# Kernel tuning notes

Hardware: AMD Instinct MI355X
Metric: run time of the kernel (lower is better)

## Reference

```python
import jax, jax.numpy as jnp
import numpy as np

SOFTCAP = 30.0

def setup_inputs() -> dict:
    key = jax.random.key(0)
    ks = jax.random.split(key, 5)
    T, D, F, E = 8192, 2048, 4096, 8
    s_in = 1.0 / np.sqrt(D)
    s_mid = 1.0 / np.sqrt(F)
    return {
        "hidden_states": jax.random.normal(ks[0], (T, D), jnp.float32),
        "gate_w": jax.random.normal(ks[1], (D, E), jnp.float32) * s_in,
        "w_gate": jax.random.normal(ks[2], (E, D, F), jnp.float32) * s_in,
        "w_up": jax.random.normal(ks[3], (E, D, F), jnp.float32) * s_in,
        "w_down": jax.random.normal(ks[4], (E, F, D), jnp.float32) * s_mid,
        "top_k": 2,
    }

def reference(hidden_states, gate_w, w_gate, w_up, w_down, top_k):
    x = hidden_states
    T = x.shape[0]
    # --- router: fp32 gate, tanh softcap, softmax ---
    logits = x.astype(jnp.float32) @ gate_w                      # [T, E]
    logits = jnp.tanh(logits / SOFTCAP) * SOFTCAP
    probs = jax.nn.softmax(logits, axis=-1)                      # [T, E]
    # --- top-k selection (weights are the softmax probs, no renorm) ---
    weights, idx = jax.lax.top_k(probs, top_k)                   # [T, k]
    combine = jnp.zeros_like(probs).at[jnp.arange(T)[:, None], idx].set(
        weights.astype(probs.dtype))                              # [T, E]
    combine = combine.astype(x.dtype)
    # --- expert MLPs: gelu(x@w_gate) * (x@w_up) @ w_down, scan over E ---
    def step(acc, ewts):
        wg, wu, wd, c = ewts                                     # [D,F],[D,F],[F,D],[T]
        h = jax.nn.gelu(x @ wg) * (x @ wu)                       # [T, F]
        return acc + c[:, None] * (h @ wd), None
    out, _ = jax.lax.scan(step, jnp.zeros_like(x),
                          (w_gate, w_up, w_down, combine.T))
    return out
```

## Files before the change

### kernel.cpp

```cpp
#include <hip/hip_runtime.h>
#include <hip/hip_bf16.h>
#include <cstdint>
#include <cstddef>

#define TNUM 8192
#define DDIM 2048
#define FDIM 4096
#define NEXP 8

typedef __attribute__((ext_vector_type(4))) float f32x4;
typedef __attribute__((ext_vector_type(4))) unsigned u32x4;
typedef __attribute__((ext_vector_type(8))) short s16x8;
typedef __attribute__((ext_vector_type(8))) __bf16 bf16x8v;

__device__ inline f32x4 mfma16(s16x8 a, s16x8 b, f32x4 c) {
  return __builtin_amdgcn_mfma_f32_16x16x32_bf16(
      __builtin_bit_cast(bf16x8v, a), __builtin_bit_cast(bf16x8v, b), c, 0, 0, 0);
}

__device__ inline unsigned short bf16r(float f) {
  union { float f; unsigned u; } x; x.f = f;
  unsigned r = x.u + 0x7fffu + ((x.u >> 16) & 1u);
  return (unsigned short)(r >> 16);
}

__device__ inline unsigned pk2(float a, float b) {
  __hip_bfloat162 h = __float22bfloat162_rn(make_float2(a, b));
  unsigned r;
  __builtin_memcpy(&r, &h, 4);
  return r;
}

__device__ inline int swz16(int row, int b) {
  return (row << 7) + (b ^ ((row & 7) << 4));
}

typedef const __attribute__((address_space(1))) void* gp_t;
typedef __attribute__((address_space(3))) void* lp_t;
__device__ inline void gl16(const void* g, void* l) {
  __builtin_amdgcn_global_load_lds((gp_t)g, (lp_t)l, 16, 0, 0);
}

#define FENCE asm volatile("" ::: "memory")

__global__ __launch_bounds__(256) void k_router(
    const float* __restrict__ x, const float* __restrict__ gw,
    int* __restrict__ top_idx, float* __restrict__ top_w, int* __restrict__ counts) {
  __shared__ float gwT[NEXP][DDIM];
  const int tid = threadIdx.x;
  for (int i = tid; i < NEXP * DDIM; i += 256) {
    int d = i >> 3, e = i & 7;
    gwT[e][d] = gw[i];
  }
  __syncthreads();
  const int lane = tid & 63;
  const int t = blockIdx.x * 4 + (tid >> 6);
  const float4* xr = (const float4*)(x + (size_t)t * DDIM);
  double acc[NEXP];
#pragma unroll
  for (int e = 0; e < NEXP; e++) acc[e] = 0.0;
  for (int d4 = lane; d4 < DDIM / 4; d4 += 64) {
    float4 xv = xr[d4];
#pragma unroll
    for (int e = 0; e < NEXP; e++) {
      float4 gv = *(const float4*)&gwT[e][d4 * 4];
      acc[e] += (double)xv.x * gv.x + (double)xv.y * gv.y +
                (double)xv.z * gv.z + (double)xv.w * gv.w;
    }
  }
#pragma unroll
  for (int e = 0; e < NEXP; e++) {
    double v = acc[e];
#pragma unroll
    for (int s = 32; s > 0; s >>= 1) v += __shfl_xor(v, s);
    acc[e] = v;
  }
  if (lane == 0) {
    int i0 = 0; double b0 = acc[0];
#pragma unroll
    for (int e = 1; e < NEXP; e++) if (acc[e] > b0) { b0 = acc[e]; i0 = e; }
    int i1 = (i0 == 0) ? 1 : 0; double b1 = acc[i1];
#pragma unroll
    for (int e = 0; e < NEXP; e++) {
      if (e == i0 || e == i1) continue;
      if (acc[e] > b1) { b1 = acc[e]; i1 = e; }
    }
    float lc[NEXP]; float mx = -1e30f;
#pragma unroll
    for (int e = 0; e < NEXP; e++) {
      lc[e] = tanhf((float)(acc[e] * (1.0 / 30.0))) * 30.0f;
      mx = lc[e] > mx ? lc[e] : mx;
    }
    float s = 0.0f;
#pragma unroll
    for (int e = 0; e < NEXP; e++) { lc[e] = expf(lc[e] - mx); s += lc[e]; }
    float inv = 1.0f / s;
    top_idx[t * 2] = i0; top_idx[t * 2 + 1] = i1;
    top_w[t * 2] = lc[i0] * inv; top_w[t * 2 + 1] = lc[i1] * inv;
    atomicAdd(&counts[i0], 1);
    atomicAdd(&counts[i1], 1);
  }
}

__global__ void k_scan(const int* __restrict__ counts, int* __restrict__ offs,
                       int* __restrict__ cursor) {
  if (threadIdx.x == 0) {
    int s = 0;
    for (int e = 0; e < NEXP; e++) { offs[e] = s; cursor[e] = s; s += counts[e]; }
    offs[NEXP] = s;
  }
}

__global__ void k_scatter(const int* __restrict__ top_idx, const float* __restrict__ top_w,
                          int* __restrict__ cursor, int* __restrict__ perm_tok,
                          float* __restrict__ perm_w) {
  int t = blockIdx.x * 256 + threadIdx.x;
#pragma unroll
  for (int k = 0; k < 2; k++) {
    int e = top_idx[t * 2 + k];
    int pos = atomicAdd(&cursor[e], 1);
    perm_tok[pos] = t;
    perm_w[pos] = top_w[t * 2 + k];
  }
}

__global__ void k_cast(const float* __restrict__ x, unsigned short* __restrict__ xb) {
  size_t i = ((size_t)blockIdx.x * 256 + threadIdx.x) * 8;
  f32x4 a = *(const f32x4*)(x + i);
  f32x4 b = *(const f32x4*)(x + i + 4);
  u32x4 v;
  v[0] = pk2(a[0], a[1]); v[1] = pk2(a[2], a[3]);
  v[2] = pk2(b[0], b[1]); v[3] = pk2(b[2], b[3]);
  *(u32x4*)(xb + i) = v;
}

__global__ __launch_bounds__(256) void k_convT(
    const float* __restrict__ src, unsigned short* __restrict__ dst,
    int K, int N, int cmap) {
  __shared__ char ct[8192];
  const int e = blockIdx.z;
  const float* src_e = src + (size_t)e * K * N;
  const int nout = cmap ? 2 * N : N;
  unsigned short* dst_e = dst + (size_t)e * nout * K;
  const int k0 = blockIdx.y * 64, n0 = blockIdx.x * 64;
  const int tid = threadIdx.x;
#pragma unroll
  for (int i = 0; i < 4; i++) {
    int idx = tid + i * 256;
    int kr = idx >> 4, f4 = idx & 15;
    f32x4 v = *(const f32x4*)(src_e + (size_t)(k0 + kr) * N + n0 + f4 * 4);
#pragma unroll
    for (int j = 0; j < 4; j++) {
      int n = f4 * 4 + j;
      *(unsigned short*)(ct + n * 128 + ((kr * 2) ^ ((n & 7) << 4))) = bf16r(v[j]);
    }
  }
  __syncthreads();
#pragma unroll
  for (int i = 0; i < 2; i++) {
    int s = tid + i * 256;
    int n = s >> 3, ks = s & 7;
    int gn = n0 + n;
    int cd = cmap ? (((gn >> 4) << 5) + (gn & 15) + (cmap == 2 ? 16 : 0)) : gn;
    s16x8 val = *(const s16x8*)(ct + n * 128 + ((ks * 16) ^ ((n & 7) << 4)));
    *(s16x8*)(dst_e + (size_t)cd * K + k0 + ks * 8) = val;
  }
}

#define PHASE(MIH, NIH, BUF)                                                   \
  {                                                                            \
    char* Ab_ = lds + (BUF) * 65536;                                           \
    char* Bb_ = Ab_ + 32768;                                                   \
    __builtin_amdgcn_s_setprio(1);                                             \
    _Pragma("unroll") for (int kk = 0; kk < 2; kk++) {                         \
      s16x8 b0_ = *(const s16x8*)(Bb_ +                                        \
          swz16(wc * 64 + (NIH) * 32 + l15, kk * 64 + lk * 16));               \
      s16x8 b1_ = *(const s16x8*)(Bb_ +                                        \
          swz16(wc * 64 + (NIH) * 32 + 16 + l15, kk * 64 + lk * 16));          \
      _Pragma("unroll") for (int mi = 0; mi < 4; mi++) {                       \
        s16x8 a_ = *(const s16x8*)(Ab_ +                                       \
            swz16(wr * 128 + (MIH) * 64 + mi * 16 + l15, kk * 64 + lk * 16));  \
        acc[(MIH) * 4 + mi][(NIH) * 2 + 0] =                                   \
            mfma16(a_, b0_, acc[(MIH) * 4 + mi][(NIH) * 2 + 0]);               \
        acc[(MIH) * 4 + mi][(NIH) * 2 + 1] =                                   \
            mfma16(a_, b1_, acc[(MIH) * 4 + mi][(NIH) * 2 + 1]);               \
      }                                                                        \
    }                                                                          \
    __builtin_amdgcn_s_setprio(0);                                             \
  }

#define STAGEU(U, TN)                                                          \
  {                                                                            \
    char* db_ = lds + ((TN) & 1) * 65536 + (U) * 16384 + wid * 2048;           \
    gl16(sp[U][0] + (size_t)(TN) * 64, db_);                                   \
    gl16(sp[U][1] + (size_t)(TN) * 64, db_ + 1024);                            \
  }

#define VMC(N) asm volatile("s_waitcnt vmcnt(" #N ")" ::: "memory")

__global__ __launch_bounds__(512, 2) void k_mlp1(
    const unsigned short* __restrict__ xb, const unsigned short* __restrict__ wguT,
    const int* __restrict__ perm_tok, const int* __restrict__ offs,
    unsigned short* __restrict__ H) {
  extern __shared__ char lds[];
  const int e = blockIdx.z;
  const int off = offs[e], cnt = offs[e + 1] - off;
  const int nb = blockIdx.x * 256;
  const unsigned short* wgu_e = wguT + (size_t)e * 2 * DDIM * FDIM;
  const int tid = threadIdx.x;
  const int lane = tid & 63;
  const int wid = tid >> 6;
  const int wr = wid >> 2, wc = wid & 3;
  const int l15 = lane & 15, lk = lane >> 4;
  const int NT = DDIM / 64;

#pragma unroll 1
  for (int mt = blockIdx.y; mt * 256 < cnt; mt += 8) {
    const unsigned short* sp[4][2];
#pragma unroll
    for (int c = 0; c < 2; c++) {
      int r = wid * 16 + c * 8 + (lane >> 3);
      int k16 = (lane & 7) ^ (r & 7);
      int glo = mt * 256 + r, ghi = mt * 256 + 128 + r;
      if (glo >= cnt) glo = cnt - 1;
      if (ghi >= cnt) ghi = cnt - 1;
      sp[0][c] = xb + (size_t)perm_tok[off + glo] * DDIM + k16 * 8;
      sp[1][c] = xb + (size_t)perm_tok[off + ghi] * DDIM + k16 * 8;
      sp[2][c] = wgu_e + (size_t)(nb + r) * DDIM + k16 * 8;
      sp[3][c] = wgu_e + (size_t)(nb + 128 + r) * DDIM + k16 * 8;
    }
    f32x4 acc[8][4];
#pragma unroll
    for (int mi = 0; mi < 8; mi++)
#pragma unroll
      for (int ni = 0; ni < 4; ni++) acc[mi][ni] = f32x4{0.f, 0.f, 0.f, 0.f};

    STAGEU(0, 0) STAGEU(1, 0) STAGEU(2, 0) STAGEU(3, 0)
    VMC(0);
    FENCE;
    __builtin_amdgcn_s_barrier();
    FENCE;
#pragma unroll 1
    for (int t = 0; t < NT; t++) {
      const int buf = t & 1;
      if (t + 1 < NT) {
        STAGEU(0, t + 1) STAGEU(1, t + 1) STAGEU(2, t + 1) STAGEU(3, t + 1)
      }
      PHASE(0, 0, buf);
      PHASE(0, 1, buf);
      PHASE(1, 0, buf);
      PHASE(1, 1, buf);
      VMC(0);
      FENCE;
      __builtin_amdgcn_s_barrier();
      FENCE;
    }

#pragma unroll
    for (int am = 0; am < 8; am++) {
      int rb = wr * 128 + am * 16 + lk * 4;
#pragma unroll
      for (int j = 0; j < 4; j++) {
        int gm = mt * 256 + rb + j;
        if (gm < cnt) {
          unsigned short* hrow = H + (size_t)(off + gm) * FDIM;
#pragma unroll
          for (int ni = 0; ni < 4; ni += 2) {
            int jj = (nb >> 4) + wc * 4 + ni;
            int hc = ((jj >> 1) << 4) + l15;
            float g = acc[am][ni][j];
            float u = acc[am][ni + 1][j];
            float x3 = g * g * g;
            float gl = 0.5f * g * (1.0f + tanhf(0.7978845608f * (g + 0.044715f * x3)));
            hrow[hc] = bf16r(gl * u);
          }
        }
      }
    }
  }
}

__global__ __launch_bounds__(512, 2) void k_mlp2(
    const unsigned short* __restrict__ H, const unsigned short* __restrict__ wdT,
    const int* __restrict__ perm_tok, const float* __restrict__ perm_w,
    const int* __restrict__ offs, float* __restrict__ out) {
  extern __shared__ char lds[];
  const int e = blockIdx.z;
  const int off = offs[e], cnt = offs[e + 1] - off;
  const int nb = blockIdx.x * 256;
  const unsigned short* wd_e = wdT + (size_t)e * FDIM * DDIM;
  const int tid = threadIdx.x;
  const int lane = tid & 63;
  const int wid = tid >> 6;
  const int wr = wid >> 2, wc = wid & 3;
  const int l15 = lane & 15, lk = lane >> 4;
  const int NT = FDIM / 64;

#pragma unroll 1
  for (int mt = blockIdx.y; mt * 256 < cnt; mt += 8) {
    const unsigned short* sp[4][2];
#pragma unroll
    for (int c = 0; c < 2; c++) {
      int r = wid * 16 + c * 8 + (lane >> 3);
      int k16 = (lane & 7) ^ (r & 7);
      int glo = mt * 256 + r, ghi = mt * 256 + 128 + r;
      if (glo >= cnt) glo = cnt - 1;
      if (ghi >= cnt) ghi = cnt - 1;
      sp[0][c] = H + (size_t)(off + glo) * FDIM + k16 * 8;
      sp[1][c] = H + (size_t)(off + ghi) * FDIM + k16 * 8;
      sp[2][c] = wd_e + (size_t)(nb + r) * FDIM + k16 * 8;
      sp[3][c] = wd_e + (size_t)(nb + 128 + r) * FDIM + k16 * 8;
    }
    f32x4 acc[8][4];
#pragma unroll
    for (int mi = 0; mi < 8; mi++)
#pragma unroll
      for (int ni = 0; ni < 4; ni++) acc[mi][ni] = f32x4{0.f, 0.f, 0.f, 0.f};

    STAGEU(0, 0) STAGEU(1, 0) STAGEU(2, 0) STAGEU(3, 0)
    VMC(0);
    FENCE;
    __builtin_amdgcn_s_barrier();
    FENCE;
#pragma unroll 1
    for (int t = 0; t < NT; t++) {
      const int buf = t & 1;
      if (t + 1 < NT) {
        STAGEU(0, t + 1) STAGEU(1, t + 1) STAGEU(2, t + 1) STAGEU(3, t + 1)
      }
      PHASE(0, 0, buf);
      PHASE(0, 1, buf);
      PHASE(1, 0, buf);
      PHASE(1, 1, buf);
      VMC(0);
      FENCE;
      __builtin_amdgcn_s_barrier();
      FENCE;
    }

#pragma unroll
    for (int am = 0; am < 8; am++) {
      int rb = wr * 128 + am * 16 + lk * 4;
#pragma unroll
      for (int j = 0; j < 4; j++) {
        int gm = mt * 256 + rb + j;
        if (gm < cnt) {
          int tok = perm_tok[off + gm];
          float w = perm_w[off + gm];
          float* orow = out + (size_t)tok * DDIM + nb + wc * 64 + l15;
#pragma unroll
          for (int ni = 0; ni < 4; ni++) atomicAdd(&orow[ni * 16], w * acc[am][ni][j]);
        }
      }
    }
  }
}

extern "C" void kernel_launch(void* const* d_in, const int* in_sizes, int n_in,
                              void* d_out, int out_size, void* d_ws, size_t ws_size,
                              hipStream_t stream) {
  const float* x = (const float*)d_in[0];
  const float* gw = (const float*)d_in[1];
  const float* wgate = (const float*)d_in[2];
  const float* wup = (const float*)d_in[3];
  const float* wdown = (const float*)d_in[4];
  float* out = (float*)d_out;

  const size_t XB_B = 33554432;
  const size_t H_B = 134217728;
  const size_t WGU_B = 268435456;
  const size_t WD_B = 134217728;

  char* ws = (char*)d_ws;
  unsigned short* xb = (unsigned short*)ws;
  unsigned short* H = (unsigned short*)(ws + XB_B);
  unsigned short* wguT = (unsigned short*)(ws + XB_B + H_B);
  unsigned short* wdT = (unsigned short*)(ws + XB_B + H_B + WGU_B);
  char* meta = ws + XB_B + H_B + WGU_B + WD_B;
  int* counts = (int*)(meta);
  int* offs = (int*)(meta + 64);
  int* cursor = (int*)(meta + 128);
  int* top_idx = (int*)(meta + 256);
  float* top_w = (float*)(meta + 256 + 65536);
  int* perm_tok = (int*)(meta + 256 + 131072);
  float* perm_w = (float*)(meta + 256 + 196608);

  (void)hipFuncSetAttribute((const void*)k_mlp1,
                            hipFuncAttributeMaxDynamicSharedMemorySize, 131072);
  (void)hipFuncSetAttribute((const void*)k_mlp2,
                            hipFuncAttributeMaxDynamicSharedMemorySize, 131072);

  (void)hipMemsetAsync(counts, 0, 64, stream);
  (void)hipMemsetAsync(d_out, 0, (size_t)TNUM * DDIM * 4, stream);
  k_router<<<TNUM / 4, 256, 0, stream>>>(x, gw, top_idx, top_w, counts);
  k_scan<<<1, 64, 0, stream>>>(counts, offs, cursor);
  k_scatter<<<TNUM / 256, 256, 0, stream>>>(top_idx, top_w, cursor, perm_tok, perm_w);
  k_cast<<<(TNUM * DDIM / 8) / 256, 256, 0, stream>>>(x, xb);
  k_convT<<<dim3(FDIM / 64, DDIM / 64, NEXP), 256, 0, stream>>>(wgate, wguT, DDIM, FDIM, 1);
  k_convT<<<dim3(FDIM / 64, DDIM / 64, NEXP), 256, 0, stream>>>(wup, wguT, DDIM, FDIM, 2);
  k_convT<<<dim3(DDIM / 64, FDIM / 64, NEXP), 256, 0, stream>>>(wdown, wdT, FDIM, DDIM, 0);
  k_mlp1<<<dim3(2 * FDIM / 256, 8, NEXP), 512, 131072, stream>>>(xb, wguT, perm_tok, offs, H);
  k_mlp2<<<dim3(DDIM / 256, 8, NEXP), 512, 131072, stream>>>(H, wdT, perm_tok, perm_w, offs, out);
}
```

Baseline: 1.555 ms.

## Interleave global prefetch staging with LDS reads and MFMA phases using per-phase barriers

Restructures the main GEMM loop in both MLP kernels into four phases. Each phase first loads all its A/B fragments from LDS, then issues one quarter of the next tile's global-to-LDS staging, hits a workgroup barrier, and runs its MFMAs at raised priority. The aim is to spread memory traffic across the compute and to synchronize waves so LDS reads and MFMA bursts interleave, in the style of ping-pong scheduling. The cost is four extra barriers per K-step and more fragment registers live at once, which could hurt occupancy or add stalls.

```diff
diff --git a/kernel.cpp b/kernel.cpp
--- a/kernel.cpp
+++ b/kernel.cpp
@@ -167,28 +167,6 @@
   }
 }
 
-#define PHASE(MIH, NIH, BUF)                                                   \
-  {                                                                            \
-    char* Ab_ = lds + (BUF) * 65536;                                           \
-    char* Bb_ = Ab_ + 32768;                                                   \
-    __builtin_amdgcn_s_setprio(1);                                             \
-    _Pragma("unroll") for (int kk = 0; kk < 2; kk++) {                         \
-      s16x8 b0_ = *(const s16x8*)(Bb_ +                                        \
-          swz16(wc * 64 + (NIH) * 32 + l15, kk * 64 + lk * 16));               \
-      s16x8 b1_ = *(const s16x8*)(Bb_ +                                        \
-          swz16(wc * 64 + (NIH) * 32 + 16 + l15, kk * 64 + lk * 16));          \
-      _Pragma("unroll") for (int mi = 0; mi < 4; mi++) {                       \
-        s16x8 a_ = *(const s16x8*)(Ab_ +                                       \
-            swz16(wr * 128 + (MIH) * 64 + mi * 16 + l15, kk * 64 + lk * 16));  \
-        acc[(MIH) * 4 + mi][(NIH) * 2 + 0] =                                   \
-            mfma16(a_, b0_, acc[(MIH) * 4 + mi][(NIH) * 2 + 0]);               \
-        acc[(MIH) * 4 + mi][(NIH) * 2 + 1] =                                   \
-            mfma16(a_, b1_, acc[(MIH) * 4 + mi][(NIH) * 2 + 1]);               \
-      }                                                                        \
-    }                                                                          \
-    __builtin_amdgcn_s_setprio(0);                                             \
-  }
-
 #define STAGEU(U, TN)                                                          \
   {                                                                            \
     char* db_ = lds + ((TN) & 1) * 65536 + (U) * 16384 + wid * 2048;           \
@@ -197,6 +175,44 @@
   }
 
 #define VMC(N) asm volatile("s_waitcnt vmcnt(" #N ")" ::: "memory")
+
+#define PH(MIH, NIH, U)                                                        \
+  {                                                                            \
+    char* Ab_ = lds + buf * 65536;                                             \
+    char* Bb_ = Ab_ + 32768;                                                   \
+    s16x8 a0_[4], a1_[4];                                                      \
+    _Pragma("unroll") for (int mi = 0; mi < 4; mi++) {                         \
+      a0_[mi] = *(const s16x8*)(Ab_ +                                          \
+          swz16(wr * 128 + (MIH) * 64 + mi * 16 + l15, lk * 16));              \
+      a1_[mi] = *(const s16x8*)(Ab_ +                                          \
+          swz16(wr * 128 + (MIH) * 64 + mi * 16 + l15, 64 + lk * 16));         \
+    }                                                                          \
+    s16x8 b00_ = *(const s16x8*)(Bb_ +                                         \
+        swz16(wc * 64 + (NIH) * 32 + l15, lk * 16));                           \
+    s16x8 b01_ = *(const s16x8*)(Bb_ +                                         \
+        swz16(wc * 64 + (NIH) * 32 + 16 + l15, lk * 16));                      \
+    s16x8 b10_ = *(const s16x8*)(Bb_ +                                         \
+        swz16(wc * 64 + (NIH) * 32 + l15, 64 + lk * 16));                      \
+    s16x8 b11_ = *(const s16x8*)(Bb_ +                                         \
+        swz16(wc * 64 + (NIH) * 32 + 16 + l15, 64 + lk * 16));                 \
+    if (more) STAGEU(U, t + 1);                                                \
+    FENCE;                                                                     \
+    __builtin_amdgcn_s_barrier();                                              \
+    __builtin_amdgcn_s_setprio(1);                                             \
+    _Pragma("unroll") for (int mi = 0; mi < 4; mi++) {                         \
+      acc[(MIH) * 4 + mi][(NIH) * 2] =                                         \
+          mfma16(a0_[mi], b00_, acc[(MIH) * 4 + mi][(NIH) * 2]);               \
+      acc[(MIH) * 4 + mi][(NIH) * 2 + 1] =                                     \
+          mfma16(a0_[mi], b01_, acc[(MIH) * 4 + mi][(NIH) * 2 + 1]);           \
+    }                                                                          \
+    _Pragma("unroll") for (int mi = 0; mi < 4; mi++) {                         \
+      acc[(MIH) * 4 + mi][(NIH) * 2] =                                         \
+          mfma16(a1_[mi], b10_, acc[(MIH) * 4 + mi][(NIH) * 2]);               \
+      acc[(MIH) * 4 + mi][(NIH) * 2 + 1] =                                     \
+          mfma16(a1_[mi], b11_, acc[(MIH) * 4 + mi][(NIH) * 2 + 1]);           \
+    }                                                                          \
+    __builtin_amdgcn_s_setprio(0);                                             \
+  }
 
 __global__ __launch_bounds__(512, 2) void k_mlp1(
     const unsigned short* __restrict__ xb, const unsigned short* __restrict__ wguT,
@@ -243,13 +259,11 @@
 #pragma unroll 1
     for (int t = 0; t < NT; t++) {
       const int buf = t & 1;
-      if (t + 1 < NT) {
-        STAGEU(0, t + 1) STAGEU(1, t + 1) STAGEU(2, t + 1) STAGEU(3, t + 1)
-      }
-      PHASE(0, 0, buf);
-      PHASE(0, 1, buf);
-      PHASE(1, 0, buf);
-      PHASE(1, 1, buf);
+      const bool more = (t + 1) < NT;
+      PH(0, 0, 0)
+      PH(0, 1, 1)
+      PH(1, 0, 2)
+      PH(1, 1, 3)
       VMC(0);
       FENCE;
       __builtin_amdgcn_s_barrier();
@@ -325,13 +339,11 @@
 #pragma unroll 1
     for (int t = 0; t < NT; t++) {
       const int buf = t & 1;
-      if (t + 1 < NT) {
-        STAGEU(0, t + 1) STAGEU(1, t + 1) STAGEU(2, t + 1) STAGEU(3, t + 1)
-      }
-      PHASE(0, 0, buf);
-      PHASE(0, 1, buf);
-      PHASE(1, 0, buf);
-      PHASE(1, 1, buf);
+      const bool more = (t + 1) < NT;
+      PH(0, 0, 0)
+      PH(0, 1, 1)
+      PH(1, 0, 2)
+      PH(1, 1, 3)
       VMC(0);
       FENCE;
       __builtin_amdgcn_s_barrier();
```

Measured after the change: 1.613 ms. +3.7%, slower.

## Split K-tile staging into half-tiles interleaved with MFMA in both expert GEMMs

Applied to the files above, without the earlier changes.

Both MLP GEMM kernels now split each 64-wide K tile into two 32-wide halves, each with its own LDS region and barrier. The next tile's A and B loads are issued between the LDS fragment reads and the MFMA bursts. The full vmcnt(0) drain per tile becomes a partial vmcnt(4) wait, and the swizzle is changed to an XOR layout with 64-byte rows. The aim is to keep global-to-LDS traffic in flight during compute and cut barrier stalls, at the cost of twice as many barriers and holding eight A fragments in registers.

```diff
diff --git a/kernel.cpp b/kernel.cpp
--- a/kernel.cpp
+++ b/kernel.cpp
@@ -29,10 +29,6 @@
   unsigned r;
   __builtin_memcpy(&r, &h, 4);
   return r;
-}
-
-__device__ inline int swz16(int row, int b) {
-  return (row << 7) + (b ^ ((row & 7) << 4));
 }
 
 typedef const __attribute__((address_space(1))) void* gp_t;
@@ -167,36 +163,47 @@
   }
 }
 
-#define PHASE(MIH, NIH, BUF)                                                   \
+#define STG_A(KK, TN)                                                          \
   {                                                                            \
-    char* Ab_ = lds + (BUF) * 65536;                                           \
-    char* Bb_ = Ab_ + 32768;                                                   \
+    char* d_ = lds + ((TN) & 1) * 65536 + (KK) * 16384 + wid * 2048;           \
+    gl16(spA[0] + (size_t)(TN) * 128 + (KK) * 64, d_);                         \
+    gl16(spA[1] + (size_t)(TN) * 128 + (KK) * 64, d_ + 1024);                  \
+  }
+#define STG_B(KK, TN)                                                          \
+  {                                                                            \
+    char* d_ = lds + ((TN) & 1) * 65536 + 32768 + (KK) * 16384 + wid * 2048;   \
+    gl16(spB[0] + (size_t)(TN) * 128 + (KK) * 64, d_);                         \
+    gl16(spB[1] + (size_t)(TN) * 128 + (KK) * 64, d_ + 1024);                  \
+  }
+
+#define VMC(N) asm volatile("s_waitcnt vmcnt(" #N ")" ::: "memory")
+
+#define RGN(KK, TN, MORE)                                                      \
+  {                                                                            \
+    char* Aq_ = lds + ((TN) & 1) * 65536 + (KK) * 16384;                       \
+    char* Bq_ = Aq_ + 32768;                                                   \
+    s16x8 a_[8];                                                               \
+    _Pragma("unroll") for (int mi = 0; mi < 8; mi++)                           \
+      a_[mi] = *(const s16x8*)(Aq_ + (wr * 128 + mi * 16 + l15) * 64 + sl16);  \
+    s16x8 b0_ = *(const s16x8*)(Bq_ + (wc * 64 + l15) * 64 + sl16);            \
+    s16x8 b1_ = *(const s16x8*)(Bq_ + (wc * 64 + 16 + l15) * 64 + sl16);       \
+    if (MORE) { STG_A(KK, (TN) + 1); }                                         \
     __builtin_amdgcn_s_setprio(1);                                             \
-    _Pragma("unroll") for (int kk = 0; kk < 2; kk++) {                         \
-      s16x8 b0_ = *(const s16x8*)(Bb_ +                                        \
-          swz16(wc * 64 + (NIH) * 32 + l15, kk * 64 + lk * 16));               \
-      s16x8 b1_ = *(const s16x8*)(Bb_ +                                        \
-          swz16(wc * 64 + (NIH) * 32 + 16 + l15, kk * 64 + lk * 16));          \
-      _Pragma("unroll") for (int mi = 0; mi < 4; mi++) {                       \
-        s16x8 a_ = *(const s16x8*)(Ab_ +                                       \
-            swz16(wr * 128 + (MIH) * 64 + mi * 16 + l15, kk * 64 + lk * 16));  \
-        acc[(MIH) * 4 + mi][(NIH) * 2 + 0] =                                   \
-            mfma16(a_, b0_, acc[(MIH) * 4 + mi][(NIH) * 2 + 0]);               \
-        acc[(MIH) * 4 + mi][(NIH) * 2 + 1] =                                   \
-            mfma16(a_, b1_, acc[(MIH) * 4 + mi][(NIH) * 2 + 1]);               \
-      }                                                                        \
+    _Pragma("unroll") for (int mi = 0; mi < 8; mi++) {                         \
+      acc[mi][0] = mfma16(a_[mi], b0_, acc[mi][0]);                            \
+      acc[mi][1] = mfma16(a_[mi], b1_, acc[mi][1]);                            \
     }                                                                          \
     __builtin_amdgcn_s_setprio(0);                                             \
-  }
-
-#define STAGEU(U, TN)                                                          \
-  {                                                                            \
-    char* db_ = lds + ((TN) & 1) * 65536 + (U) * 16384 + wid * 2048;           \
-    gl16(sp[U][0] + (size_t)(TN) * 64, db_);                                   \
-    gl16(sp[U][1] + (size_t)(TN) * 64, db_ + 1024);                            \
-  }
-
-#define VMC(N) asm volatile("s_waitcnt vmcnt(" #N ")" ::: "memory")
+    s16x8 b2_ = *(const s16x8*)(Bq_ + (wc * 64 + 32 + l15) * 64 + sl16);       \
+    s16x8 b3_ = *(const s16x8*)(Bq_ + (wc * 64 + 48 + l15) * 64 + sl16);       \
+    if (MORE) { STG_B(KK, (TN) + 1); }                                         \
+    __builtin_amdgcn_s_setprio(1);                                             \
+    _Pragma("unroll") for (int mi = 0; mi < 8; mi++) {                         \
+      acc[mi][2] = mfma16(a_[mi], b2_, acc[mi][2]);                            \
+      acc[mi][3] = mfma16(a_[mi], b3_, acc[mi][3]);                            \
+    }                                                                          \
+    __builtin_amdgcn_s_setprio(0);                                             \
+  }
 
 __global__ __launch_bounds__(512, 2) void k_mlp1(
     const unsigned short* __restrict__ xb, const unsigned short* __restrict__ wguT,
@@ -212,22 +219,21 @@
   const int wid = tid >> 6;
   const int wr = wid >> 2, wc = wid & 3;
   const int l15 = lane & 15, lk = lane >> 4;
+  const int sl16 = (lk ^ ((l15 >> 1) & 3)) * 16;
+  const int g16 = ((lane & 3) ^ ((lane >> 3) & 3)) * 16;
   const int NT = DDIM / 64;
 
 #pragma unroll 1
   for (int mt = blockIdx.y; mt * 256 < cnt; mt += 8) {
-    const unsigned short* sp[4][2];
+    const char* spA[2];
+    const char* spB[2];
 #pragma unroll
     for (int c = 0; c < 2; c++) {
-      int r = wid * 16 + c * 8 + (lane >> 3);
-      int k16 = (lane & 7) ^ (r & 7);
-      int glo = mt * 256 + r, ghi = mt * 256 + 128 + r;
-      if (glo >= cnt) glo = cnt - 1;
-      if (ghi >= cnt) ghi = cnt - 1;
-      sp[0][c] = xb + (size_t)perm_tok[off + glo] * DDIM + k16 * 8;
-      sp[1][c] = xb + (size_t)perm_tok[off + ghi] * DDIM + k16 * 8;
-      sp[2][c] = wgu_e + (size_t)(nb + r) * DDIM + k16 * 8;
-      sp[3][c] = wgu_e + (size_t)(nb + 128 + r) * DDIM + k16 * 8;
+      int r = wid * 32 + c * 16 + (lane >> 2);
+      int gm = mt * 256 + r;
+      if (gm >= cnt) gm = cnt - 1;
+      spA[c] = (const char*)(xb + (size_t)perm_tok[off + gm] * DDIM) + g16;
+      spB[c] = (const char*)(wgu_e + (size_t)(nb + r) * DDIM) + g16;
     }
     f32x4 acc[8][4];
 #pragma unroll
@@ -235,25 +241,20 @@
 #pragma unroll
       for (int ni = 0; ni < 4; ni++) acc[mi][ni] = f32x4{0.f, 0.f, 0.f, 0.f};
 
-    STAGEU(0, 0) STAGEU(1, 0) STAGEU(2, 0) STAGEU(3, 0)
-    VMC(0);
-    FENCE;
-    __builtin_amdgcn_s_barrier();
-    FENCE;
+    STG_A(0, 0) STG_B(0, 0) STG_A(1, 0) STG_B(1, 0)
 #pragma unroll 1
     for (int t = 0; t < NT; t++) {
-      const int buf = t & 1;
-      if (t + 1 < NT) {
-        STAGEU(0, t + 1) STAGEU(1, t + 1) STAGEU(2, t + 1) STAGEU(3, t + 1)
-      }
-      PHASE(0, 0, buf);
-      PHASE(0, 1, buf);
-      PHASE(1, 0, buf);
-      PHASE(1, 1, buf);
-      VMC(0);
+      const bool more = (t + 1) < NT;
+      VMC(4);
       FENCE;
       __builtin_amdgcn_s_barrier();
       FENCE;
+      RGN(0, t, more)
+      if (more) { VMC(4); } else { VMC(0); }
+      FENCE;
+      __builtin_amdgcn_s_barrier();
+      FENCE;
+      RGN(1, t, more)
     }
 
 #pragma unroll
@@ -294,22 +295,21 @@
   const int wid = tid >> 6;
   const int wr = wid >> 2, wc = wid & 3;
   const int l15 = lane & 15, lk = lane >> 4;
+  const int sl16 = (lk ^ ((l15 >> 1) & 3)) * 16;
+  const int g16 = ((lane & 3) ^ ((lane >> 3) & 3)) * 16;
   const int NT = FDIM / 64;
 
 #pragma unroll 1
   for (int mt = blockIdx.y; mt * 256 < cnt; mt += 8) {
-    const unsigned short* sp[4][2];
+    const char* spA[2];
+    const char* spB[2];
 #pragma unroll
     for (int c = 0; c < 2; c++) {
-      int r = wid * 16 + c * 8 + (lane >> 3);
-      int k16 = (lane & 7) ^ (r & 7);
-      int glo = mt * 256 + r, ghi = mt * 256 + 128 + r;
-      if (glo >= cnt) glo = cnt - 1;
-      if (ghi >= cnt) ghi = cnt - 1;
-      sp[0][c] = H + (size_t)(off + glo) * FDIM + k16 * 8;
-      sp[1][c] = H + (size_t)(off + ghi) * FDIM + k16 * 8;
-      sp[2][c] = wd_e + (size_t)(nb + r) * FDIM + k16 * 8;
-      sp[3][c] = wd_e + (size_t)(nb + 128 + r) * FDIM + k16 * 8;
+      int r = wid * 32 + c * 16 + (lane >> 2);
+      int gm = mt * 256 + r;
+      if (gm >= cnt) gm = cnt - 1;
+      spA[c] = (const char*)(H + (size_t)(off + gm) * FDIM) + g16;
+      spB[c] = (const char*)(wd_e + (size_t)(nb + r) * FDIM) + g16;
     }
     f32x4 acc[8][4];
 #pragma unroll
@@ -317,25 +317,20 @@
 #pragma unroll
       for (int ni = 0; ni < 4; ni++) acc[mi][ni] = f32x4{0.f, 0.f, 0.f, 0.f};
 
-    STAGEU(0, 0) STAGEU(1, 0) STAGEU(2, 0) STAGEU(3, 0)
-    VMC(0);
-    FENCE;
-    __builtin_amdgcn_s_barrier();
-    FENCE;
+    STG_A(0, 0) STG_B(0, 0) STG_A(1, 0) STG_B(1, 0)
 #pragma unroll 1
     for (int t = 0; t < NT; t++) {
-      const int buf = t & 1;
-      if (t + 1 < NT) {
-        STAGEU(0, t + 1) STAGEU(1, t + 1) STAGEU(2, t + 1) STAGEU(3, t + 1)
-      }
-      PHASE(0, 0, buf);
-      PHASE(0, 1, buf);
-      PHASE(1, 0, buf);
-      PHASE(1, 1, buf);
-      VMC(0);
+      const bool more = (t + 1) < NT;
+      VMC(4);
       FENCE;
       __builtin_amdgcn_s_barrier();
       FENCE;
+      RGN(0, t, more)
+      if (more) { VMC(4); } else { VMC(0); }
+      FENCE;
+      __builtin_amdgcn_s_barrier();
+      FENCE;
+      RGN(1, t, more)
     }
 
 #pragma unroll
```

Result: faster. 1.468 ms (-5.6%).
